# Kernel optimization log

Measured on AMD Instinct MI355X. Metric: run time of the kernel, lower is better.

Reference implementation:

```python
import math
import jax, jax.numpy as jnp
import numpy as np

N_HEAD = 16
ROPE_BASE = 10000.0


def _rope_tables(T, half, dtype):
    # build_sin_cos(seq_len, dim=head_dim//2): inv freq of length `half`
    pos = jnp.arange(T, dtype=jnp.float32)[:, None]                      # [T,1]
    inv = jnp.exp(jnp.arange(0, half * 2, 2, dtype=jnp.float32) * (-math.log(ROPE_BASE) / (half * 2)))  # [half]
    ang = pos * inv                                                       # [T,half]
    return jnp.sin(ang).astype(dtype), jnp.cos(ang).astype(dtype)


def setup_inputs() -> dict:
    key = jax.random.key(0)
    k1, k2, k3 = jax.random.split(key, 3)
    B, T, C = 2, 2048, 2048
    x = jax.random.normal(k1, (B, T, C), dtype=jnp.float32)
    w_qkv = jax.random.normal(k2, (3 * C, C), dtype=jnp.float32) * (1.0 / math.sqrt(C))
    w_proj = jax.random.normal(k3, (C, C), dtype=jnp.float32) * (1.0 / math.sqrt(C))
    return {"x": x, "w_qkv": w_qkv, "w_proj": w_proj}


def reference(x, w_qkv, w_proj):
    B, T, C = x.shape
    H = N_HEAD
    D = C // H
    half = D // 2

    qkv = jnp.einsum('btc,fc->btf', x, w_qkv).reshape(B, T, 3, H, D)
    q, k, v = qkv[:, :, 0], qkv[:, :, 1], qkv[:, :, 2]   # [B,T,H,D]

    sin, cos = _rope_tables(T, half, x.dtype)            # [T,half]
    sin = sin[None, :, None, :]                          # [1,T,1,half]
    cos = cos[None, :, None, :]

    def rot(t):
        t1, t2 = t[..., :half], t[..., half:]
        return jnp.concatenate([t1 * cos - t2 * sin, t2 * cos + t1 * sin], axis=-1)

    q, k = rot(q), rot(k)

    scale = 1.0 / math.sqrt(D)
    scores = jnp.einsum('bthd,bshd->bhts', q, k) * scale  # [B,H,T,T]
    causal = jnp.tril(jnp.ones((T, T), dtype=bool))
    scores = jnp.where(causal[None, None], scores, jnp.finfo(scores.dtype).min)
    probs = jax.nn.softmax(scores, axis=-1)
    out = jnp.einsum('bhts,bshd->bhtd', probs, v)         # [B,H,T,D]

    # Faithful to torch: view(B,T,H,D).permute(0,2,1,3).reshape_as(x)
    # flash output is token-major (B,T,H,D); permute gives (B,H,T,D), then flat reshape to (B,T,C).
    out = out.reshape(B, T, C)
    return jnp.einsum('btc,oc->bto', out, w_proj)
```

## Files before the change

kernel.cpp:

```cpp
#include <hip/hip_runtime.h>
#include <math.h>

typedef __attribute__((ext_vector_type(8))) short short8;
typedef __attribute__((ext_vector_type(4))) float f32x4;
typedef __attribute__((ext_vector_type(16))) float f32x16;
typedef __attribute__((ext_vector_type(4))) unsigned short ushort4v;
typedef __attribute__((ext_vector_type(2))) int int2v;

#define AS1 __attribute__((address_space(1)))
#define AS3 __attribute__((address_space(3)))
#define GLOAD16(src, dst) __builtin_amdgcn_global_load_lds((const AS1 void*)(src), (AS3 void*)(dst), 16, 0, 0)
#define VMWAIT(N) asm volatile("s_waitcnt vmcnt(" #N ")" ::: "memory")
#define LGKM0()   asm volatile("s_waitcnt lgkmcnt(0)" ::: "memory")

__device__ __forceinline__ unsigned short f2b(float f) {
    union { float f; unsigned int u; } c; c.f = f;
    return (unsigned short)((c.u + 0x7FFFu + ((c.u >> 16) & 1u)) >> 16);
}
__device__ __forceinline__ float b2f(unsigned short u) {
    union { unsigned int u; float f; } c; c.u = ((unsigned int)u) << 16;
    return c.f;
}
__device__ __forceinline__ int cvt_pk_bf16(float a, float b) {
    int r;
    asm("v_cvt_pk_bf16_f32 %0, %1, %2" : "=v"(r) : "v"(a), "v"(b));
    return r;
}
__device__ __forceinline__ int xcd_swz(int id, int nwg) {
    int q = nwg >> 3, r = nwg & 7, x = id & 7, rest = id >> 3;
    return (x < r ? x * (q + 1) : r * (q + 1) + (x - r) * q) + rest;
}

__global__ void cvt2(const float* __restrict__ a, const float* __restrict__ bsrc,
                     unsigned short* __restrict__ dst, int n4a) {
    int f = blockIdx.x * 256 + threadIdx.x;
    float4 v = (f < n4a) ? ((const float4*)a)[f] : ((const float4*)bsrc)[f - n4a];
    ushort4v o;
    o.x = f2b(v.x); o.y = f2b(v.y); o.z = f2b(v.z); o.w = f2b(v.w);
    ((ushort4v*)dst)[f] = o;
}

__global__ __launch_bounds__(256) void mid_fused(unsigned short* __restrict__ qkv,
                                                 unsigned short* __restrict__ vtg,
                                                 const float* __restrict__ wproj,
                                                 unsigned short* __restrict__ wpb) {
    int bid = blockIdx.x;
    if (bid < 16384) {
        int tid = bid * 256 + threadIdx.x;
        int i = tid & 63;
        int h = (tid >> 6) & 15;
        int t = (tid >> 10) & 2047;
        int b = tid >> 21;
        float inv = __expf((float)i * -0.14391156608f);
        float ang = (float)t * inv;
        float sn = sinf(ang), cs = cosf(ang);
        size_t base0 = ((size_t)(((b << 11) + t) * 3)) << 11;
#pragma unroll
        for (int s = 0; s < 2; ++s) {
            size_t base = base0 + (size_t)s * 2048 + (h << 7);
            float v1 = b2f(qkv[base + i]);
            float v2 = b2f(qkv[base + 64 + i]);
            qkv[base + i]      = f2b(v1 * cs - v2 * sn);
            qkv[base + 64 + i] = f2b(v2 * cs + v1 * sn);
        }
    } else if (bid < 16384 + 4096) {
        int flat = (bid - 16384) * 256 + threadIdx.x;
        int t = flat & 2047;
        int dc = (flat >> 11) & 15;
        int h = (flat >> 15) & 15;
        int b = flat >> 19;
        short8 v = *(const short8*)(qkv + ((size_t)(b * 2048 + t) * 3 + 2) * 2048 + h * 128 + dc * 8);
        size_t base = ((size_t)(b * 16 + h) * 128 + dc * 8) * 2048 + t;
#pragma unroll
        for (int j = 0; j < 8; j++) vtg[base + (size_t)j * 2048] = (unsigned short)v[j];
    } else {
        int f = (bid - 20480) * 256 + threadIdx.x;
#pragma unroll
        for (int r = 0; r < 4; ++r, f += 1024 * 256) {
            float4 v = ((const float4*)wproj)[f];
            ushort4v o;
            o.x = f2b(v.x); o.y = f2b(v.y); o.z = f2b(v.z); o.w = f2b(v.w);
            ((ushort4v*)wpb)[f] = o;
        }
    }
}

template<int OUT_BF16>
__global__ __launch_bounds__(256) void gemm_nt(const unsigned short* __restrict__ A,
                                               const unsigned short* __restrict__ B,
                                               void* __restrict__ Cout,
                                               int N, int K) {
    constexpr int BK = 64;
    __shared__ unsigned short lA[128 * BK];
    __shared__ unsigned short lB[128 * BK];
    int tid = threadIdx.x;
    int lane = tid & 63, w = tid >> 6;
    int wr = w >> 1, wc = w & 1;
    int col = lane & 15, lg = lane >> 4;
    int nwg = gridDim.x * gridDim.y;
    int id = xcd_swz(blockIdx.y * gridDim.x + blockIdx.x, nwg);
    int rowBase = (id / gridDim.x) * 128;
    int colBase = (id % gridDim.x) * 128;
    f32x4 acc[4][4];
#pragma unroll
    for (int m = 0; m < 4; m++)
#pragma unroll
        for (int n = 0; n < 4; n++) acc[m][n] = (f32x4){0.f, 0.f, 0.f, 0.f};

    int rowS[4], scb[4];
#pragma unroll
    for (int it = 0; it < 4; ++it) {
        int d = it * 4096 + tid * 16;
        int row = d >> 7;
        int cb = d & 127;
        rowS[it] = row;
        scb[it] = cb ^ ((row & 7) << 4);
    }

    for (int kk = 0; kk < K; kk += BK) {
        __syncthreads();
#pragma unroll
        for (int it = 0; it < 4; ++it) {
            const char* srcA = (const char*)A + ((size_t)(rowBase + rowS[it]) * K + kk) * 2 + scb[it];
            const char* srcB = (const char*)B + ((size_t)(colBase + rowS[it]) * K + kk) * 2 + scb[it];
            char* dA = (char*)lA + it * 4096 + w * 1024;
            char* dB = (char*)lB + it * 4096 + w * 1024;
            GLOAD16(srcA, dA);
            GLOAD16(srcB, dB);
        }
        __syncthreads();
#pragma unroll
        for (int kc = 0; kc < 2; ++kc) {
            int cbyte = kc * 64 + 16 * lg;
            short8 af[4], bf[4];
#pragma unroll
            for (int m = 0; m < 4; m++) {
                int row = wr * 64 + m * 16 + col;
                af[m] = *(const short8*)((const char*)lA + row * 128 + (cbyte ^ ((row & 7) << 4)));
            }
#pragma unroll
            for (int n = 0; n < 4; n++) {
                int row = wc * 64 + n * 16 + col;
                bf[n] = *(const short8*)((const char*)lB + row * 128 + (cbyte ^ ((row & 7) << 4)));
            }
#pragma unroll
            for (int m = 0; m < 4; m++)
#pragma unroll
                for (int n = 0; n < 4; n++)
                    acc[m][n] = __builtin_amdgcn_mfma_f32_16x16x32_bf16(af[m], bf[n], acc[m][n], 0, 0, 0);
        }
    }
    int rbase = 4 * lg;
#pragma unroll
    for (int m = 0; m < 4; m++)
#pragma unroll
        for (int reg = 0; reg < 4; ++reg) {
            int r = rowBase + wr * 64 + m * 16 + rbase + reg;
#pragma unroll
            for (int n = 0; n < 4; n++) {
                int c = colBase + wc * 64 + n * 16 + col;
                float v = acc[m][n][reg];
                if (OUT_BF16) ((unsigned short*)Cout)[(size_t)r * N + c] = f2b(v);
                else          ((float*)Cout)[(size_t)r * N + c] = v;
            }
        }
}

__global__ __launch_bounds__(256, 2) void attn_fused(const unsigned short* __restrict__ qkv,
                                                     const unsigned short* __restrict__ vtg,
                                                     unsigned short* __restrict__ out) {
    constexpr int T = 2048;
    __shared__ unsigned short Kl[3][64 * 128];
    int tid = threadIdx.x, lane = tid & 63, w = tid >> 6;
    int q = lane & 31, hi = lane >> 5;
    int id = blockIdx.x;
    int i0 = id & 1, u = (id >> 1) & 127, i8 = id >> 8;
    int bh = (u >> 4) | (i0 << 3) | (i8 << 4);
    int b = bh >> 4, h = bh & 15;
    int v4 = u & 15;
    int qt = (i0 ^ i8) ? (15 - v4) : v4;
    int qbase = qt * 128;
    int nkv = 2 * qt + 2;
    int tq = qbase + w * 32 + q;
    const float sc2 = 0.08838834764831845f * 1.44269504088896340f;

    short8 qf[8];
    {
        const unsigned short* qp = qkv + ((size_t)(b * T + tq) * 3) * 2048 + h * 128;
#pragma unroll
        for (int s = 0; s < 8; s++) qf[s] = *(const short8*)(qp + s * 16 + hi * 8);
    }
    f32x16 O[4];
#pragma unroll
    for (int dt = 0; dt < 4; dt++)
#pragma unroll
        for (int r = 0; r < 16; r++) O[dt][r] = 0.f;
    float m = -1e30f, l = 0.f;

    auto stageK = [&](int t) {
        int tt = t < nkv ? t : nkv - 1;
        int kvb = tt * 64;
        char* Kb = (char*)&Kl[t % 3][0];
#pragma unroll
        for (int it = 0; it < 4; ++it) {
            int dby = it * 4096 + tid * 16;
            int row = dby >> 8, cb = dby & 255;
            int scb = cb ^ ((row & 7) << 4);
            const char* src = (const char*)qkv + (((size_t)(b * T + kvb + row) * 3 + 1) * 2048 + h * 128) * 2 + scb;
            GLOAD16(src, Kb + it * 4096 + w * 1024);
        }
    };

    stageK(0); stageK(1);
    const unsigned short* vbase = vtg + (size_t)bh * 128 * 2048;

    for (int kv = 0; kv < nkv; ++kv) {
        if (kv == 0)      { VMWAIT(4); }
        else if (kv == 1) { VMWAIT(20); }
        else              { VMWAIT(36); }
        stageK(kv + 2);
        int kvbase = kv * 64;
        bool act = kvbase < qbase + (w + 1) * 32;
        const char* Kb = (const char*)&Kl[kv % 3][0];
        if (act) {
            short8 vf[4][4];
#pragma unroll
            for (int dt = 0; dt < 4; dt++) {
                int d = dt * 32 + q;
#pragma unroll
                for (int ks = 0; ks < 4; ks++)
                    vf[dt][ks] = *(const short8*)(vbase + (size_t)d * 2048 + kvbase + ks * 16 + hi * 8);
            }
            f32x16 p0, p1;
#pragma unroll
            for (int r = 0; r < 16; r++) { p0[r] = 0.f; p1[r] = 0.f; }
            __builtin_amdgcn_s_setprio(1);
#pragma unroll
            for (int s = 0; s < 8; s++) {
                int cb = s * 32 + hi * 16;
                short8 k0 = *(const short8*)(Kb + q * 256 + (cb ^ ((q & 7) << 4)));
                p0 = __builtin_amdgcn_mfma_f32_32x32x16_bf16(k0, qf[s], p0, 0, 0, 0);
                short8 k1 = *(const short8*)(Kb + (32 + q) * 256 + (cb ^ ((q & 7) << 4)));
                p1 = __builtin_amdgcn_mfma_f32_32x32x16_bf16(k1, qf[s], p1, 0, 0, 0);
            }
            __builtin_amdgcn_s_setprio(0);
#pragma unroll
            for (int r = 0; r < 16; r++) { p0[r] *= sc2; p1[r] *= sc2; }
            bool diag = (kvbase + 63 > qbase + w * 32);
            if (diag) {
#pragma unroll
                for (int r = 0; r < 16; r++) {
                    int kg = kvbase + (r & 3) + 8 * (r >> 2) + 4 * hi;
                    if (kg > tq) p0[r] = -3e38f;
                    if (kg + 32 > tq) p1[r] = -3e38f;
                }
            }
            float mx = -3e38f;
#pragma unroll
            for (int r = 0; r < 16; r++) mx = fmaxf(mx, fmaxf(p0[r], p1[r]));
            mx = fmaxf(mx, __shfl_xor(mx, 32));
            if (!__all(mx - m <= 8.0f)) {
                float mn = fmaxf(m, mx);
                float esc = exp2f(m - mn);
                m = mn;
                l *= esc;
#pragma unroll
                for (int dt = 0; dt < 4; dt++)
#pragma unroll
                    for (int r = 0; r < 16; r++) O[dt][r] *= esc;
            }
            float rs = 0.f;
#pragma unroll
            for (int r = 0; r < 16; r++) {
                p0[r] = exp2f(p0[r] - m); rs += p0[r];
                p1[r] = exp2f(p1[r] - m); rs += p1[r];
            }
            rs += __shfl_xor(rs, 32);
            l += rs;
            union Frag { int i[4]; short8 s; } pa[4];
#pragma unroll
            for (int g = 0; g < 4; g++) {
                float e[8];
#pragma unroll
                for (int j = 0; j < 8; j++) e[j] = (g < 2) ? p0[(g & 1) * 8 + j] : p1[(g & 1) * 8 + j];
                int a0 = cvt_pk_bf16(e[0], e[1]);
                int a1 = cvt_pk_bf16(e[2], e[3]);
                int b0 = cvt_pk_bf16(e[4], e[5]);
                int b1 = cvt_pk_bf16(e[6], e[7]);
                int s0 = hi ? a0 : b0; int r0 = __shfl_xor(s0, 32);
                int s1 = hi ? a1 : b1; int r1 = __shfl_xor(s1, 32);
                pa[g].i[0] = hi ? r0 : a0;
                pa[g].i[1] = hi ? r1 : a1;
                pa[g].i[2] = hi ? b0 : r0;
                pa[g].i[3] = hi ? b1 : r1;
            }
            __builtin_amdgcn_s_setprio(1);
#pragma unroll
            for (int dt = 0; dt < 4; dt++)
#pragma unroll
                for (int ks = 0; ks < 4; ks++)
                    O[dt] = __builtin_amdgcn_mfma_f32_32x32x16_bf16(vf[dt][ks], pa[ks].s, O[dt], 0, 0, 0);
            __builtin_amdgcn_s_setprio(0);
        }
        LGKM0();
        __builtin_amdgcn_s_barrier();
    }
    float linv = 1.0f / l;
    size_t obase = ((size_t)bh * T + tq) * 128;
#pragma unroll
    for (int dt = 0; dt < 4; dt++)
#pragma unroll
        for (int g = 0; g < 4; g++) {
            int d0 = dt * 32 + g * 8 + 4 * hi;
            int w0 = cvt_pk_bf16(O[dt][4 * g + 0] * linv, O[dt][4 * g + 1] * linv);
            int w1 = cvt_pk_bf16(O[dt][4 * g + 2] * linv, O[dt][4 * g + 3] * linv);
            int2v o; o[0] = w0; o[1] = w1;
            *(int2v*)(out + obase + d0) = o;
        }
}

extern "C" void kernel_launch(void* const* d_in, const int* in_sizes, int n_in,
                              void* d_out, int out_size, void* d_ws, size_t ws_size,
                              hipStream_t stream) {
    const float* x      = (const float*)d_in[0];
    const float* w_qkv  = (const float*)d_in[1];
    const float* w_proj = (const float*)d_in[2];
    const int B = 2, T = 2048, C = 2048;
    const int M = B * T;
    const int F = 3 * C;

    size_t need = ((size_t)M * C + (size_t)F * C + (size_t)M * F) * 2;
    if (ws_size < need) return;
    unsigned short* rX  = (unsigned short*)d_ws;
    unsigned short* rW  = rX + (size_t)M * C;
    unsigned short* rQ  = rW + (size_t)F * C;
    unsigned short* rVT = rW;
    unsigned short* rWp = rW + (size_t)B * 16 * 128 * T;

    cvt2<<<(M * C + F * C) / 1024, 256, 0, stream>>>(x, w_qkv, rX, (M * C) / 4);
    gemm_nt<1><<<dim3(F / 128, M / 128), 256, 0, stream>>>(rX, rW, (void*)rQ, F, C);
    mid_fused<<<16384 + 4096 + 1024, 256, 0, stream>>>(rQ, rVT, w_proj, rWp);
    attn_fused<<<512, 256, 0, stream>>>(rQ, rVT, rX);
    gemm_nt<0><<<dim3(C / 128, M / 128), 256, 0, stream>>>(rX, rWp, d_out, C, C);
}
```

Measured before the change: 328.9 us.

## Stage V tiles into LDS with double-buffered async global-to-LDS loads

Each wave used to load its own copy of the V tile for every KV step straight from global memory into registers. Now the whole block loads the 128x64 V tile once into a double-buffered, XOR-swizzled shared-memory buffer with global_load_lds, and waves read their V fragments from LDS right before each PV MFMA. This removes the redundant per-wave global/L2 reads and the register pressure of holding the V fragments. In exchange it adds LDS usage and LDS read traffic, and replaces the old staged vmcnt waits with a single uniform wait. There is no barrier between that wait and the reads of the current V buffer, so completion of V loads issued by other waves may not be guaranteed.

```diff
diff --git a/kernel.cpp b/kernel.cpp
--- a/kernel.cpp
+++ b/kernel.cpp
@@ -171,6 +171,7 @@
                                                      unsigned short* __restrict__ out) {
     constexpr int T = 2048;
     __shared__ unsigned short Kl[3][64 * 128];
+    __shared__ unsigned short Vl[2][128 * 64];
     int tid = threadIdx.x, lane = tid & 63, w = tid >> 6;
     int q = lane & 31, hi = lane >> 5;
     int id = blockIdx.x;
@@ -210,27 +211,31 @@
             GLOAD16(src, Kb + it * 4096 + w * 1024);
         }
     };
-
-    stageK(0); stageK(1);
-    const unsigned short* vbase = vtg + (size_t)bh * 128 * 2048;
+    auto stageV = [&](int t) {
+        int tt = t < nkv ? t : nkv - 1;
+        int kvb = tt * 64;
+        char* Vb = (char*)&Vl[t & 1][0];
+#pragma unroll
+        for (int it = 0; it < 4; ++it) {
+            int dby = it * 4096 + tid * 16;
+            int d = dby >> 7, cb = dby & 127;
+            int scb = cb ^ ((d & 7) << 4);
+            const char* src = (const char*)vtg + (((size_t)bh * 128 + d) * 2048 + kvb) * 2 + scb;
+            GLOAD16(src, Vb + it * 4096 + w * 1024);
+        }
+    };
+
+    stageK(0); stageV(0); stageK(1);
 
     for (int kv = 0; kv < nkv; ++kv) {
-        if (kv == 0)      { VMWAIT(4); }
-        else if (kv == 1) { VMWAIT(20); }
-        else              { VMWAIT(36); }
         stageK(kv + 2);
+        stageV(kv + 1);
+        VMWAIT(8);
         int kvbase = kv * 64;
         bool act = kvbase < qbase + (w + 1) * 32;
         const char* Kb = (const char*)&Kl[kv % 3][0];
+        const char* Vb = (const char*)&Vl[kv & 1][0];
         if (act) {
-            short8 vf[4][4];
-#pragma unroll
-            for (int dt = 0; dt < 4; dt++) {
-                int d = dt * 32 + q;
-#pragma unroll
-                for (int ks = 0; ks < 4; ks++)
-                    vf[dt][ks] = *(const short8*)(vbase + (size_t)d * 2048 + kvbase + ks * 16 + hi * 8);
-            }
             f32x16 p0, p1;
 #pragma unroll
             for (int r = 0; r < 16; r++) { p0[r] = 0.f; p1[r] = 0.f; }
@@ -296,10 +301,14 @@
             }
             __builtin_amdgcn_s_setprio(1);
 #pragma unroll
-            for (int dt = 0; dt < 4; dt++)
-#pragma unroll
-                for (int ks = 0; ks < 4; ks++)
-                    O[dt] = __builtin_amdgcn_mfma_f32_32x32x16_bf16(vf[dt][ks], pa[ks].s, O[dt], 0, 0, 0);
+            for (int dt = 0; dt < 4; dt++) {
+                int d = dt * 32 + q;
+#pragma unroll
+                for (int ks = 0; ks < 4; ks++) {
+                    short8 vfr = *(const short8*)(Vb + d * 128 + ((ks * 32 + hi * 16) ^ ((d & 7) << 4)));
+                    O[dt] = __builtin_amdgcn_mfma_f32_32x32x16_bf16(vfr, pa[ks].s, O[dt], 0, 0, 0);
+                }
+            }
             __builtin_amdgcn_s_setprio(0);
         }
         LGKM0();
```

New measurement: 288.3 us. -12.3%, faster.
